# Kernel optimization log

Measured on AMD Instinct MI355X. Metric: run time of the kernel, lower is better.

## Reference

```python
import jax, jax.numpy as jnp
import numpy as np

B, N, E, D, M, T, P, HS, HN, C, NH = 64, 1024, 512, 1024, 16, 12, 2048, 2048, 64, 4, 8
EPS = 1e-8


def _ln(x, g, b):
    m = x.mean(-1, keepdims=True)
    v = ((x - m) ** 2).mean(-1, keepdims=True)
    return (x - m) / jnp.sqrt(v + 1e-5) * g + b


def _glu(x):
    a, b = jnp.split(x, 2, axis=-1)
    return a * jax.nn.sigmoid(b)


def setup_inputs() -> dict:
    key = jax.random.key(0)
    ks = jax.random.split(key, 24)
    s = 0.02
    rn = lambda k, sh: jax.random.normal(k, sh, jnp.float32) * s
    inp = {
        'kv_tokens': jax.random.normal(ks[0], (B, N, E), jnp.float32),
        'raw_r_act': jnp.full((P,), -10.0, jnp.float32),  # no_decay_init
        'raw_r_out': jnp.full((P,), -10.0, jnp.float32),
        'q_w': rn(ks[1], (E, P)), 'q_b': jnp.zeros((E,), jnp.float32),
        'in_proj_w': rn(ks[2], (3 * E, E)), 'in_proj_b': jnp.zeros((3 * E,), jnp.float32),
        'out_proj_w': rn(ks[3], (E, E)), 'out_proj_b': jnp.zeros((E,), jnp.float32),
        'z_ln_g': jnp.ones((D,), jnp.float32), 'z_ln_b': jnp.zeros((D,), jnp.float32),
        'o_ln_g': jnp.ones((E,), jnp.float32), 'o_ln_b': jnp.zeros((E,), jnp.float32),
        'gate_w': rn(ks[4], (D, D + E)), 'gate_b': jnp.zeros((D,), jnp.float32),
        'cand_w': rn(ks[5], (D, D + E)), 'cand_b': jnp.zeros((D,), jnp.float32),
        'syn1_w': rn(ks[6], (HS, D + E)), 'syn1_b': jnp.zeros((HS,), jnp.float32),
        'syn2_w': rn(ks[7], (D, HS)), 'syn2_b': jnp.zeros((D,), jnp.float32),
        'nlm1_w': rn(ks[8], (D, M, 2 * HN)), 'nlm1_b': jnp.zeros((D, 2 * HN), jnp.float32),
        'nlm2_w': rn(ks[9], (D, HN, 2)), 'nlm2_b': jnp.zeros((D, 2), jnp.float32),
        'head_w': rn(ks[10], (C, P)), 'head_b': jnp.zeros((C,), jnp.float32),
        'act_left': jax.random.randint(ks[11], (P,), 0, D),
        'act_right': jax.random.randint(ks[12], (P,), 0, D),
        'out_left': jax.random.randint(ks[13], (P,), 0, D),
        'out_right': jax.random.randint(ks[14], (P,), 0, D),
    }
    return inp


def reference(kv_tokens, raw_r_act, raw_r_out, q_w, q_b, in_proj_w, in_proj_b,
              out_proj_w, out_proj_b, z_ln_g, z_ln_b, o_ln_g, o_ln_b,
              gate_w, gate_b, cand_w, cand_b, syn1_w, syn1_b, syn2_w, syn2_b,
              nlm1_w, nlm1_b, nlm2_w, nlm2_b, head_w, head_b,
              act_left, act_right, out_left, out_right):
    dh = E // NH
    scale = 1.0 / np.sqrt(dh).astype(np.float32)
    Wq, Wk, Wv = jnp.split(in_proj_w, 3, axis=0)
    bq, bk, bv = jnp.split(in_proj_b, 3, axis=0)
    # K/V are tick-invariant: project once.
    k = (kv_tokens @ Wk.T + bk).reshape(B, N, NH, dh).transpose(0, 2, 1, 3)  # [B,H,N,dh]
    v = (kv_tokens @ Wv.T + bv).reshape(B, N, NH, dh).transpose(0, 2, 1, 3)
    decay_a = jnp.exp(-jax.nn.softplus(raw_r_act))[None, :]
    decay_o = jnp.exp(-jax.nn.softplus(raw_r_out))[None, :]

    z0 = jnp.zeros((B, D), kv_tokens.dtype)
    A0 = jnp.zeros((B, D, M), kv_tokens.dtype)
    # init_state with z0 == 0 -> alpha 0, beta 1, synch 0
    a_a0 = z0[:, act_left] * z0[:, act_right]
    b_a0 = jnp.ones_like(a_a0)
    s_a0 = a_a0 / jnp.sqrt(b_a0 + EPS)
    a_o0 = z0[:, out_left] * z0[:, out_right]
    b_o0 = jnp.ones_like(a_o0)

    def tick(carry, _):
        z, A, a_a, b_a, s_a, a_o, b_o = carry
        # attention query from action sync
        q = s_a @ q_w.T + q_b                                  # [B,E]
        qh = (q @ Wq.T + bq).reshape(B, NH, 1, dh)
        scores = jnp.einsum('bhqd,bhnd->bhqn', qh, k) * scale  # [B,H,1,N]
        attn = jax.nn.softmax(scores, axis=-1)
        o = jnp.einsum('bhqn,bhnd->bhqd', attn, v).reshape(B, E)
        o = o @ out_proj_w.T + out_proj_b
        o = _ln(o, o_ln_g, o_ln_b)                             # LN on o
        zn = _ln(z, z_ln_g, z_ln_b)                            # LN on z
        # gated fusion
        u = jnp.concatenate([zn, o], axis=-1)
        g = jax.nn.sigmoid(u @ gate_w.T + gate_b)
        h = jnp.tanh(u @ cand_w.T + cand_b)
        z_bar = (1.0 - g) * zn + g * h
        fused = jnp.concatenate([z_bar, o], axis=-1)           # [B,D+E]
        # synapse MLP -> pre-activation
        pre = jax.nn.gelu(fused @ syn1_w.T + syn1_b, approximate=False) @ syn2_w.T + syn2_b
        A = jnp.concatenate([A[:, :, 1:], pre[:, :, None]], axis=-1)  # shift history
        # deep NLM (per-neuron SuperLinear + GLU, twice)
        h1 = _glu(jnp.einsum('bdm,dmh->bdh', A, nlm1_w) + nlm1_b)
        z = _glu(jnp.einsum('bdh,dho->bdo', h1, nlm2_w) + nlm2_b)[..., 0]
        # decayed pair synchronisation updates
        a_a = decay_a * a_a + z[:, act_left] * z[:, act_right]
        b_a = decay_a * b_a + 1.0
        s_a = a_a / jnp.sqrt(b_a + EPS)
        a_o = decay_o * a_o + z[:, out_left] * z[:, out_right]
        b_o = decay_o * b_o + 1.0
        s_o = a_o / jnp.sqrt(b_o + EPS)
        logits = s_o @ head_w.T + head_b                       # [B,C]
        return (z, A, a_a, b_a, s_a, a_o, b_o), (logits, z)

    carry0 = (z0, A0, a_a0, b_a0, s_a0, a_o0, b_o0)
    _, (logits_t, z_t) = jax.lax.scan(tick, carry0, None, length=T)
    logits_ticks = jnp.transpose(logits_t, (1, 2, 0))          # [B,C,T]
    p = jnp.clip(jax.nn.softmax(logits_ticks, axis=1), 1e-8, None)
    ent = -(p * jnp.log(p)).sum(axis=1)
    certainty = 1.0 - ent / np.float32(np.log(C))              # [B,T]
    z_ticks = jnp.transpose(z_t, (1, 0, 2))                    # [B,T,D]
    return logits_ticks, certainty, z_ticks
```

## Files before the change

### kernel.cpp

```cpp
#include <hip/hip_runtime.h>
#include <hip/hip_bf16.h>

#define B_ 64
#define N_ 1024
#define E_ 512
#define D_ 1024
#define M_ 16
#define T_ 12
#define P_ 2048
#define HS_ 2048
#define HN_ 64
#define C_ 4
#define NH_ 8
#define DH_ 64

typedef __attribute__((ext_vector_type(8))) short bf16x8;
typedef __attribute__((ext_vector_type(4))) float f32x4;

__device__ __forceinline__ float bf2f(unsigned int u) {
    union { unsigned int i; float f; } c; c.i = (u & 0xffffu) << 16; return c.f;
}
__device__ __forceinline__ unsigned short f2bf(float f) {
    union { float f; unsigned int i; } c; c.f = f;
    unsigned int x = c.i;
    unsigned int r = x + 0x7fffu + ((x >> 16) & 1u);
    return (unsigned short)(r >> 16);
}

__global__ void init_kernel(unsigned short* s_a_bf, float* a_a, float* a_o, float* z) {
    int i = blockIdx.x * 256 + threadIdx.x;
    if (i < B_ * P_) { a_a[i] = 0.f; a_o[i] = 0.f; s_a_bf[i] = 0; }
    if (i < B_ * D_) z[i] = 0.f;
}

__global__ __launch_bounds__(256) void decay_prep_kernel(const float* __restrict__ raw_a,
                                                         const float* __restrict__ raw_o,
                                                         float* __restrict__ da, float* __restrict__ dz,
                                                         float* __restrict__ invsa, float* __restrict__ invso) {
    int p = blockIdx.x * 256 + threadIdx.x;
    if (p < P_) {
        float a = 1.f / (1.f + expf(raw_a[p]));
        float o = 1.f / (1.f + expf(raw_o[p]));
        da[p] = a; dz[p] = o;
        float ba = 1.f, bo = 1.f;
        for (int t = 0; t < T_; t++) {
            ba = a * ba + 1.f;
            bo = o * bo + 1.f;
            invsa[t * P_ + p] = 1.0f / sqrtf(ba + 1e-8f);
            invso[t * P_ + p] = 1.0f / sqrtf(bo + 1e-8f);
        }
    }
}

__global__ __launch_bounds__(256) void cvt_bf16_kernel(const float* __restrict__ in,
                                                       unsigned short* __restrict__ out, int n4) {
    int i = blockIdx.x * 256 + threadIdx.x;
    if (i < n4) {
        float4 v = ((const float4*)in)[i];
        ushort4 o;
        o.x = f2bf(v.x); o.y = f2bf(v.y); o.z = f2bf(v.z); o.w = f2bf(v.w);
        ((ushort4*)out)[i] = o;
    }
}

__global__ __launch_bounds__(256) void cvt_all_kernel(
    const float* s0, unsigned short* d0, int n0,
    const float* s1, unsigned short* d1, int n1,
    const float* s2, unsigned short* d2, int n2,
    const float* s3, unsigned short* d3, int n3,
    const float* s4, unsigned short* d4, int n4,
    const float* s5, unsigned short* d5, int n5) {
    int total = n0 + n1 + n2 + n3 + n4 + n5;
    for (int i = blockIdx.x * 256 + threadIdx.x; i < total; i += gridDim.x * 256) {
        const float* s; unsigned short* d; int j = i;
        if (j < n0) { s = s0; d = d0; }
        else { j -= n0;
        if (j < n1) { s = s1; d = d1; }
        else { j -= n1;
        if (j < n2) { s = s2; d = d2; }
        else { j -= n2;
        if (j < n3) { s = s3; d = d3; }
        else { j -= n3;
        if (j < n4) { s = s4; d = d4; }
        else { j -= n4; s = s5; d = d5; } } } } }
        float4 v = ((const float4*)s)[j];
        ushort4 o;
        o.x = f2bf(v.x); o.y = f2bf(v.y); o.z = f2bf(v.z); o.w = f2bf(v.w);
        ((ushort4*)d)[j] = o;
    }
}

__global__ __launch_bounds__(256) void cvt_ilv_kernel(const float* __restrict__ g,
                                                      const float* __restrict__ c,
                                                      unsigned short* __restrict__ out) {
    int r = blockIdx.x;
    const float* src = (r & 1) ? (c + (size_t)(r >> 1) * 1536) : (g + (size_t)(r >> 1) * 1536);
    for (int k = threadIdx.x * 4; k < 1536; k += 1024) {
        float4 v = *(const float4*)(src + k);
        ushort4 o;
        o.x = f2bf(v.x); o.y = f2bf(v.y); o.z = f2bf(v.z); o.w = f2bf(v.w);
        *(ushort4*)(out + (size_t)r * 1536 + k) = o;
    }
}

__global__ __launch_bounds__(256) void transpose_cvt_kernel(const float* __restrict__ in,
                                                            unsigned short* __restrict__ out,
                                                            int R, int Ccols) {
    __shared__ float tb[32][33];
    int c0 = blockIdx.x * 32, r0 = blockIdx.y * 32;
    int tx = threadIdx.x & 31, ty = threadIdx.x >> 5;
#pragma unroll
    for (int i = 0; i < 32; i += 8) tb[ty + i][tx] = in[(size_t)(r0 + ty + i) * Ccols + c0 + tx];
    __syncthreads();
#pragma unroll
    for (int i = 0; i < 32; i += 8) out[(size_t)(c0 + ty + i) * R + r0 + tx] = f2bf(tb[tx][ty + i]);
}

__global__ __launch_bounds__(256) void bcomb_kernel(const float* __restrict__ in_proj_w,
                                                    const float* __restrict__ in_proj_b,
                                                    const float* __restrict__ q_b,
                                                    float* __restrict__ bc) {
    int e = blockIdx.x * 256 + threadIdx.x;
    if (e < E_) {
        const float* wr = in_proj_w + (size_t)e * E_;
        float s = in_proj_b[e];
        for (int k = 0; k < E_; k += 4) {
            float4 w4 = *(const float4*)(wr + k);
            float4 q4 = *(const float4*)(q_b + k);
            s += w4.x * q4.x + w4.y * q4.y + w4.z * q4.z + w4.w * q4.w;
        }
        bc[e] = s;
    }
}

__global__ __launch_bounds__(256) void br_kernel(const float* __restrict__ in_proj_w,
                                                 const float* __restrict__ bc,
                                                 float* __restrict__ br) {
    int g = blockIdx.x * 256 + threadIdx.x;
    int h = g >> 9, j = g & 511;
    const float* Wk = in_proj_w + (size_t)E_ * E_;
    float s = 0.f;
    for (int e = 0; e < 64; e++) {
        s += Wk[(size_t)(h * 64 + e) * E_ + j] * bc[h * 64 + e];
    }
    br[g] = s;
}

template <bool HAS_BIAS>
__global__ __launch_bounds__(256) void gemm_bt_kernel(const unsigned short* __restrict__ A,
                                                      const unsigned short* __restrict__ Bt,
                                                      const float* __restrict__ bias,
                                                      unsigned short* __restrict__ C,
                                                      int M, int N, int K) {
    __shared__ __align__(16) unsigned short ldsA[2][4096];
    __shared__ __align__(16) unsigned short ldsB[2][4096];
    int id = blockIdx.y * gridDim.x + blockIdx.x;
    int nwg = gridDim.x * gridDim.y;
    int swz = (id & 7) * (nwg >> 3) + (id >> 3);
    int bx = swz % gridDim.x, by = swz / gridDim.x;
    int m0 = by * 128;
    int n0 = bx * 128;
    int tid = threadIdx.x;
    int wv = tid >> 6, l = tid & 63;
    int wr = wv >> 1, wc = wv & 1;
    int lr = l & 15, lg = l >> 4;
    f32x4 acc[4][4] = {};

    auto stage = [&](int buf, int kt) {
        int k0 = kt * 32;
#pragma unroll
        for (int i = 0; i < 2; i++) {
            int tsk = tid + 256 * i;
            int r = tsk >> 2, g = tsk & 3;
            int gs = (g ^ (r & 3)) * 8;
            __builtin_amdgcn_global_load_lds(
                (const __attribute__((address_space(1))) void*)(A + (size_t)(m0 + r) * K + k0 + gs),
                (__attribute__((address_space(3))) void*)&ldsA[buf][tsk * 8], 16, 0, 0);
        }
#pragma unroll
        for (int i = 0; i < 2; i++) {
            int tsk = tid + 256 * i;
            int r = tsk >> 2, g = tsk & 3;
            int gs = (g ^ (r & 3)) * 8;
            __builtin_amdgcn_global_load_lds(
                (const __attribute__((address_space(1))) void*)(Bt + (size_t)(n0 + r) * K + k0 + gs),
                (__attribute__((address_space(3))) void*)&ldsB[buf][tsk * 8], 16, 0, 0);
        }
    };

    int nt = K >> 5;
    stage(0, 0);
    for (int t = 0; t < nt; t++) {
        int cur = t & 1;
        if (t + 1 < nt) {
            stage(cur ^ 1, t + 1);
            asm volatile("s_waitcnt vmcnt(4)" ::: "memory");
        } else {
            asm volatile("s_waitcnt vmcnt(0)" ::: "memory");
        }
        __builtin_amdgcn_s_barrier();
        bf16x8 af[4], bfr[4];
#pragma unroll
        for (int mi = 0; mi < 4; mi++) {
            int r = wr * 64 + mi * 16 + lr;
            af[mi] = *(const bf16x8*)&ldsA[cur][r * 32 + ((lg ^ (r & 3)) << 3)];
        }
#pragma unroll
        for (int ni = 0; ni < 4; ni++) {
            int c = wc * 64 + ni * 16 + lr;
            bfr[ni] = *(const bf16x8*)&ldsB[cur][c * 32 + ((lg ^ (c & 3)) << 3)];
        }
#pragma unroll
        for (int mi = 0; mi < 4; mi++)
#pragma unroll
            for (int ni = 0; ni < 4; ni++)
                acc[mi][ni] = __builtin_amdgcn_mfma_f32_16x16x32_bf16(af[mi], bfr[ni], acc[mi][ni], 0, 0, 0);
        __builtin_amdgcn_s_barrier();
    }
#pragma unroll
    for (int ni = 0; ni < 4; ni++) {
        int col = n0 + wc * 64 + ni * 16 + lr;
        float bv = HAS_BIAS ? bias[col] : 0.0f;
#pragma unroll
        for (int mi = 0; mi < 4; mi++) {
            int row = m0 + wr * 64 + mi * 16 + lg * 4;
#pragma unroll
            for (int r = 0; r < 4; r++) {
                C[(size_t)(row + r) * N + col] = f2bf(acc[mi][ni][r] + bv);
            }
        }
    }
}

__global__ __launch_bounds__(256) void gemm_hb_kernel(const unsigned short* __restrict__ A0, int lda, size_t sAz,
                                                      const unsigned short* __restrict__ B0, int ldb, size_t sBz,
                                                      unsigned short* __restrict__ C0, int ldc, size_t sCz,
                                                      int K) {
    __shared__ __align__(16) unsigned short ldsA[2][4096];
    __shared__ __align__(16) unsigned short ldsB[2][4096];
    const unsigned short* A = A0 + blockIdx.z * sAz;
    const unsigned short* Bt = B0 + blockIdx.z * sBz;
    unsigned short* C = C0 + blockIdx.z * sCz;
    int m0 = blockIdx.y * 128, n0 = blockIdx.x * 128;
    int tid = threadIdx.x;
    int wv = tid >> 6, l = tid & 63;
    int wr = wv >> 1, wc = wv & 1;
    int lr = l & 15, lg = l >> 4;
    f32x4 acc[4][4] = {};

    auto stage = [&](int buf, int kt) {
        int k0 = kt * 32;
#pragma unroll
        for (int i = 0; i < 2; i++) {
            int tsk = tid + 256 * i;
            int r = tsk >> 2, g = tsk & 3;
            int gs = (g ^ (r & 3)) * 8;
            __builtin_amdgcn_global_load_lds(
                (const __attribute__((address_space(1))) void*)(A + (size_t)(m0 + r) * lda + k0 + gs),
                (__attribute__((address_space(3))) void*)&ldsA[buf][tsk * 8], 16, 0, 0);
        }
#pragma unroll
        for (int i = 0; i < 2; i++) {
            int tsk = tid + 256 * i;
            int r = tsk >> 2, g = tsk & 3;
            int gs = (g ^ (r & 3)) * 8;
            __builtin_amdgcn_global_load_lds(
                (const __attribute__((address_space(1))) void*)(Bt + (size_t)(n0 + r) * ldb + k0 + gs),
                (__attribute__((address_space(3))) void*)&ldsB[buf][tsk * 8], 16, 0, 0);
        }
    };

    int nt = K >> 5;
    stage(0, 0);
    for (int t = 0; t < nt; t++) {
        int cur = t & 1;
        if (t + 1 < nt) {
            stage(cur ^ 1, t + 1);
            asm volatile("s_waitcnt vmcnt(4)" ::: "memory");
        } else {
            asm volatile("s_waitcnt vmcnt(0)" ::: "memory");
        }
        __builtin_amdgcn_s_barrier();
        bf16x8 af[4], bfr[4];
#pragma unroll
        for (int mi = 0; mi < 4; mi++) {
            int r = wr * 64 + mi * 16 + lr;
            af[mi] = *(const bf16x8*)&ldsA[cur][r * 32 + ((lg ^ (r & 3)) << 3)];
        }
#pragma unroll
        for (int ni = 0; ni < 4; ni++) {
            int c = wc * 64 + ni * 16 + lr;
            bfr[ni] = *(const bf16x8*)&ldsB[cur][c * 32 + ((lg ^ (c & 3)) << 3)];
        }
#pragma unroll
        for (int mi = 0; mi < 4; mi++)
#pragma unroll
            for (int ni = 0; ni < 4; ni++)
                acc[mi][ni] = __builtin_amdgcn_mfma_f32_16x16x32_bf16(af[mi], bfr[ni], acc[mi][ni], 0, 0, 0);
        __builtin_amdgcn_s_barrier();
    }
#pragma unroll
    for (int ni = 0; ni < 4; ni++) {
        int col = n0 + wc * 64 + ni * 16 + lr;
#pragma unroll
        for (int mi = 0; mi < 4; mi++) {
            int row = m0 + wr * 64 + mi * 16 + lg * 4;
#pragma unroll
            for (int r = 0; r < 4; r++) {
                C[(size_t)(row + r) * ldc + col] = f2bf(acc[mi][ni][r]);
            }
        }
    }
}

template <int EPI>
__global__ __launch_bounds__(256) void gemmNK_kernel(const unsigned short* __restrict__ A,
                                                     const unsigned short* __restrict__ W,
                                                     const float* __restrict__ bias0,
                                                     const float* __restrict__ bias1,
                                                     const float* __restrict__ zn32,
                                                     void* __restrict__ outp,
                                                     int N, int K) {
    __shared__ __align__(16) unsigned short ldsA[4][2][2048];
    __shared__ __align__(16) unsigned short ldsB[4][2][512];
    int n0 = blockIdx.x * 16;
    int tid = threadIdx.x;
    int w = tid >> 6, l = tid & 63;
    int Kw = K >> 2;
    int kb = w * Kw;
    int lr = l & 15, lg = l >> 4;
    int ar = l >> 2, ag = l & 3;
    f32x4 acc[4] = {};

    auto stage = [&](int buf, int kt) {
        int k0 = kb + (kt << 5);
#pragma unroll
        for (int i = 0; i < 4; i++) {
            int row = i * 16 + ar;
            int gs = (ag ^ (row & 3)) << 3;
            __builtin_amdgcn_global_load_lds(
                (const __attribute__((address_space(1))) void*)(A + (size_t)row * K + k0 + gs),
                (__attribute__((address_space(3))) void*)&ldsA[w][buf][i * 512 + l * 8], 16, 0, 0);
        }
        {
            int col = ar;
            int gs = (ag ^ (col & 3)) << 3;
            __builtin_amdgcn_global_load_lds(
                (const __attribute__((address_space(1))) void*)(W + (size_t)(n0 + col) * K + k0 + gs),
                (__attribute__((address_space(3))) void*)&ldsB[w][buf][l * 8], 16, 0, 0);
        }
    };

    int nt = Kw >> 5;
    stage(0, 0);
    for (int t = 0; t < nt; t++) {
        int cur = t & 1;
        if (t + 1 < nt) {
            stage(cur ^ 1, t + 1);
            asm volatile("s_waitcnt vmcnt(5)" ::: "memory");
        } else {
            asm volatile("s_waitcnt vmcnt(0)" ::: "memory");
        }
        bf16x8 bf = *(const bf16x8*)&ldsB[w][cur][lr * 32 + ((lg ^ (lr & 3)) << 3)];
#pragma unroll
        for (int mi = 0; mi < 4; mi++) {
            int rr = mi * 16 + lr;
            bf16x8 af = *(const bf16x8*)&ldsA[w][cur][rr * 32 + ((lg ^ (rr & 3)) << 3)];
            acc[mi] = __builtin_amdgcn_mfma_f32_16x16x32_bf16(af, bf, acc[mi], 0, 0, 0);
        }
    }
    __syncthreads();
    float* red = (float*)&ldsA[0][0][0];
#pragma unroll
    for (int mi = 0; mi < 4; mi++) {
        int row = mi * 16 + lg * 4;
#pragma unroll
        for (int q = 0; q < 4; q++) red[w * 1024 + (row + q) * 16 + lr] = acc[mi][q];
    }
    __syncthreads();
    int b = tid >> 2, c4 = (tid & 3) << 2;
    f32x4 s = *(f32x4*)&red[b * 16 + c4];
#pragma unroll
    for (int ww = 1; ww < 4; ww++) {
        f32x4 v = *(f32x4*)&red[ww * 1024 + b * 16 + c4];
        s[0] += v[0]; s[1] += v[1]; s[2] += v[2]; s[3] += v[3];
    }
    int col = n0 + c4;
    if (EPI == 0) {
        unsigned short* out = (unsigned short*)outp;
        ushort4 o;
        o.x = f2bf(0.125f * (s[0] + bias0[col + 0]));
        o.y = f2bf(0.125f * (s[1] + bias0[col + 1]));
        o.z = f2bf(0.125f * (s[2] + bias0[col + 2]));
        o.w = f2bf(0.125f * (s[3] + bias0[col + 3]));
        *(ushort4*)(out + (size_t)b * N + col) = o;
    } else if (EPI == 1) {
        float* out = (float*)outp;
        *(f32x4*)(out + (size_t)b * N + col) = s;
    } else if (EPI == 2) {
        unsigned short* out = (unsigned short*)outp;
        int j0 = col >> 1;
#pragma unroll
        for (int pp = 0; pp < 2; pp++) {
            int j = j0 + pp;
            float g = 1.0f / (1.0f + expf(-(s[pp * 2] + bias0[j])));
            float h = tanhf(s[pp * 2 + 1] + bias1[j]);
            float zb = (1.0f - g) * zn32[(size_t)b * D_ + j] + g * h;
            out[(size_t)b * 1536 + j] = f2bf(zb);
        }
    } else if (EPI == 3) {
        unsigned short* out = (unsigned short*)outp;
        ushort4 o;
#pragma unroll
        for (int j = 0; j < 4; j++) {
            float pre = s[j] + bias0[col + j];
            float val = 0.5f * pre * (1.0f + erff(pre * 0.70710678118654752f));
            ((unsigned short*)&o)[j] = f2bf(val);
        }
        *(ushort4*)(out + (size_t)b * N + col) = o;
    } else {
        float* out = (float*)outp;
#pragma unroll
        for (int j = 0; j < 4; j++) {
            out[(size_t)(col + j) * 64 + b] = s[j] + bias0[col + j];
        }
    }
}

__global__ __launch_bounds__(256) void scoreX_kernel(const unsigned short* __restrict__ X,
                                                     const unsigned short* __restrict__ r_bf,
                                                     float* __restrict__ S) {
    int b = blockIdx.y;
    int n0 = blockIdx.x * 128;
    int tid = threadIdx.x;
    int wv = tid >> 6, l = tid & 63;
    int lr = l & 15, lg = l >> 4;
    const unsigned short* Xb = X + ((size_t)b * 1024 + n0) * 512;
    const unsigned short* rb = r_bf + (size_t)b * 4096 + (size_t)(lr & 7) * 512 + lg * 8;
    f32x4 acc[2] = {};
#pragma unroll
    for (int kt = 0; kt < 16; kt++) {
        int k0 = kt * 32;
        bf16x8 bfrag = *(const bf16x8*)(rb + k0);
#pragma unroll
        for (int mi = 0; mi < 2; mi++) {
            int row = (wv * 2 + mi) * 16 + lr;
            bf16x8 afrag = *(const bf16x8*)(Xb + (size_t)row * 512 + k0 + lg * 8);
            acc[mi] = __builtin_amdgcn_mfma_f32_16x16x32_bf16(afrag, bfrag, acc[mi], 0, 0, 0);
        }
    }
    if (lr < 8) {
#pragma unroll
        for (int mi = 0; mi < 2; mi++) {
            int rowbase = (wv * 2 + mi) * 16 + lg * 4;
#pragma unroll
            for (int q = 0; q < 4; q++) {
                S[((size_t)b * 8 + lr) * 1024 + n0 + rowbase + q] = acc[mi][q];
            }
        }
    }
}

__global__ __launch_bounds__(256) void attnV_kernel(const float* __restrict__ S,
                                                    const unsigned short* __restrict__ vbuf,
                                                    unsigned short* __restrict__ o_bf) {
    int bh = blockIdx.x;
    int b = bh >> 3, h = bh & 7;
    __shared__ float sc[N_];
    __shared__ float red[8];
    __shared__ float opart[4][DH_];
    int tid = threadIdx.x;
    int w = tid >> 6, lane = tid & 63;
    const float* Ss = S + ((size_t)b * 8 + h) * 1024;
    float myv[4];
#pragma unroll
    for (int i = 0; i < 4; i++) myv[i] = Ss[tid + i * 256];
    float m = fmaxf(fmaxf(myv[0], myv[1]), fmaxf(myv[2], myv[3]));
#pragma unroll
    for (int off = 32; off >= 1; off >>= 1) m = fmaxf(m, __shfl_xor(m, off, 64));
    if (lane == 0) red[w] = m;
    __syncthreads();
    m = fmaxf(fmaxf(red[0], red[1]), fmaxf(red[2], red[3]));
    float s = 0.f;
#pragma unroll
    for (int i = 0; i < 4; i++) {
        float e = expf(myv[i] - m);
        sc[tid + i * 256] = e;
        s += e;
    }
#pragma unroll
    for (int off = 32; off >= 1; off >>= 1) s += __shfl_xor(s, off, 64);
    if (lane == 0) red[4 + w] = s;
    __syncthreads();
    float inv = 1.0f / (red[4] + red[5] + red[6] + red[7]);
    const unsigned short* vb = vbuf + (size_t)b * 1024 * 512 + h * DH_;
    int ng = lane >> 4, d4 = (lane & 15) << 2;
    float a0 = 0.f, a1 = 0.f, a2 = 0.f, a3 = 0.f;
    int n0 = w * 256;
    for (int i = 0; i < 64; i++) {
        int n = n0 + i * 4 + ng;
        uint2 pv = *(const uint2*)(vb + (size_t)n * 512 + d4);
        float sv = sc[n];
        a0 += sv * bf2f(pv.x);
        a1 += sv * bf2f(pv.x >> 16);
        a2 += sv * bf2f(pv.y);
        a3 += sv * bf2f(pv.y >> 16);
    }
    a0 += __shfl_xor(a0, 16, 64); a0 += __shfl_xor(a0, 32, 64);
    a1 += __shfl_xor(a1, 16, 64); a1 += __shfl_xor(a1, 32, 64);
    a2 += __shfl_xor(a2, 16, 64); a2 += __shfl_xor(a2, 32, 64);
    a3 += __shfl_xor(a3, 16, 64); a3 += __shfl_xor(a3, 32, 64);
    if (lane < 16) {
        opart[w][d4 + 0] = a0;
        opart[w][d4 + 1] = a1;
        opart[w][d4 + 2] = a2;
        opart[w][d4 + 3] = a3;
    }
    __syncthreads();
    if (tid < DH_) {
        float r = (opart[0][tid] + opart[1][tid] + opart[2][tid] + opart[3][tid]) * inv;
        o_bf[(size_t)b * E_ + h * DH_ + tid] = f2bf(r);
    }
}

__global__ __launch_bounds__(256) void reduce_oln_kernel(const float* __restrict__ opre,
                                                         const float* __restrict__ bout,
                                                         const float* __restrict__ og,
                                                         const float* __restrict__ obv,
                                                         const float* __restrict__ z,
                                                         const float* __restrict__ zg,
                                                         const float* __restrict__ zbv,
                                                         unsigned short* __restrict__ u_bf,
                                                         unsigned short* __restrict__ fused_bf,
                                                         float* __restrict__ zn32) {
    int b = blockIdx.x, tid = threadIdx.x;
    __shared__ float red[16];
    float v[2];
#pragma unroll
    for (int i = 0; i < 2; i++) {
        int e = tid + i * 256;
        v[i] = opre[(size_t)b * E_ + e] + bout[e];
    }
    int w = tid >> 6, lane = tid & 63;
    float s1 = v[0] + v[1];
    float s2 = v[0] * v[0] + v[1] * v[1];
#pragma unroll
    for (int off = 32; off >= 1; off >>= 1) { s1 += __shfl_xor(s1, off, 64); s2 += __shfl_xor(s2, off, 64); }
    if (lane == 0) { red[w] = s1; red[4 + w] = s2; }
    __syncthreads();
    s1 = red[0] + red[1] + red[2] + red[3];
    s2 = red[4] + red[5] + red[6] + red[7];
    float mean = s1 * (1.0f / 512.0f);
    float var = s2 * (1.0f / 512.0f) - mean * mean;
    float rstd = 1.0f / sqrtf(var + 1e-5f);
#pragma unroll
    for (int i = 0; i < 2; i++) {
        int e = tid + i * 256;
        unsigned short val = f2bf((v[i] - mean) * rstd * og[e] + obv[e]);
        u_bf[(size_t)b * 1536 + D_ + e] = val;
        fused_bf[(size_t)b * 1536 + D_ + e] = val;
    }
    float zl[4];
    float t1 = 0.f, t2 = 0.f;
#pragma unroll
    for (int i = 0; i < 4; i++) {
        int d = tid + i * 256;
        zl[i] = z[(size_t)b * D_ + d];
        t1 += zl[i]; t2 += zl[i] * zl[i];
    }
#pragma unroll
    for (int off = 32; off >= 1; off >>= 1) { t1 += __shfl_xor(t1, off, 64); t2 += __shfl_xor(t2, off, 64); }
    __syncthreads();
    if (lane == 0) { red[8 + w] = t1; red[12 + w] = t2; }
    __syncthreads();
    t1 = red[8] + red[9] + red[10] + red[11];
    t2 = red[12] + red[13] + red[14] + red[15];
    float zmean = t1 * (1.0f / 1024.0f);
    float zvar = t2 * (1.0f / 1024.0f) - zmean * zmean;
    float zr = 1.0f / sqrtf(zvar + 1e-5f);
#pragma unroll
    for (int i = 0; i < 4; i++) {
        int d = tid + i * 256;
        float zn = (zl[i] - zmean) * zr * zg[d] + zbv[d];
        u_bf[(size_t)b * 1536 + d] = f2bf(zn);
        zn32[(size_t)b * D_ + d] = zn;
    }
}

template <int NT>
__global__ __launch_bounds__(256) void nlm_kernel(const float* __restrict__ AbufT,
                                                  const unsigned short* __restrict__ w1g_bf,
                                                  const float* __restrict__ b1g,
                                                  const float* __restrict__ w2g,
                                                  const float* __restrict__ b2g,
                                                  float* __restrict__ z,
                                                  float* __restrict__ zt) {
    __shared__ float w1s[4][2048];
    __shared__ float b1s[4][128];
    __shared__ float w2s[4][128];
    __shared__ float b2s[4][2];
    int tid = threadIdx.x;
    int w = tid >> 6, lane = tid & 63;
    int d = blockIdx.x * 4 + w;
    for (int i = lane * 2; i < 2048; i += 128) {
        unsigned int pk = *(const unsigned int*)(w1g_bf + (size_t)d * 2048 + i);
        w1s[w][i] = bf2f(pk);
        w1s[w][i + 1] = bf2f(pk >> 16);
    }
    for (int i = lane; i < 128; i += 64) {
        b1s[w][i] = b1g[(size_t)d * 128 + i];
        w2s[w][i] = w2g[(size_t)d * 128 + i];
    }
    if (lane < 2) b2s[w][lane] = b2g[d * 2 + lane];
    __syncthreads();
    const int b = lane;
    float av[NT];
#pragma unroll
    for (int s = 0; s < NT; s++) av[s] = AbufT[((size_t)s * D_ + d) * 64 + b];
    constexpr int moff = M_ - NT;
    float o0 = b2s[w][0], o1 = b2s[w][1];
    for (int hh = 0; hh < 64; hh++) {
        float a = b1s[w][hh], bb = b1s[w][hh + 64];
#pragma unroll
        for (int s = 0; s < NT; s++) {
            float x = av[s];
            a += x * w1s[w][(s + moff) * 128 + hh];
            bb += x * w1s[w][(s + moff) * 128 + hh + 64];
        }
        float z1 = a / (1.0f + expf(-bb));
        o0 += z1 * w2s[w][hh * 2];
        o1 += z1 * w2s[w][hh * 2 + 1];
    }
    float zv = o0 / (1.0f + expf(-o1));
    z[(size_t)b * D_ + d] = zv;
    zt[((size_t)b * T_ + (NT - 1)) * D_ + d] = zv;
}

__global__ __launch_bounds__(256) void synchead_kernel(const float* __restrict__ z,
                                                       const int* __restrict__ act_l, const int* __restrict__ act_r,
                                                       const int* __restrict__ out_l, const int* __restrict__ out_r,
                                                       const float* __restrict__ da, const float* __restrict__ dz,
                                                       const float* __restrict__ invsa_t, const float* __restrict__ invso_t,
                                                       const float* __restrict__ head_w, const float* __restrict__ head_b,
                                                       float* __restrict__ a_a,
                                                       unsigned short* __restrict__ s_a_bf,
                                                       float* __restrict__ a_o,
                                                       float* __restrict__ out_logits, float* __restrict__ out_cert, int t) {
    int b = blockIdx.x, tid = threadIdx.x;
    __shared__ float zv[D_];
    __shared__ float red[4][4];
    for (int i = tid; i < D_; i += 256) zv[i] = z[(size_t)b * D_ + i];
    __syncthreads();
    float l0 = 0.f, l1 = 0.f, l2 = 0.f, l3 = 0.f;
    for (int p = tid; p < P_; p += 256) {
        size_t ip = (size_t)b * P_ + p;
        float aa = da[p] * a_a[ip] + zv[act_l[p]] * zv[act_r[p]];
        a_a[ip] = aa;
        s_a_bf[(size_t)b * P_ + p] = f2bf(aa * invsa_t[p]);
        float ao = dz[p] * a_o[ip] + zv[out_l[p]] * zv[out_r[p]];
        a_o[ip] = ao;
        float so = ao * invso_t[p];
        l0 += so * head_w[p];
        l1 += so * head_w[P_ + p];
        l2 += so * head_w[2 * P_ + p];
        l3 += so * head_w[3 * P_ + p];
    }
    int w = tid >> 6, lane = tid & 63;
#pragma unroll
    for (int off = 32; off >= 1; off >>= 1) {
        l0 += __shfl_xor(l0, off, 64);
        l1 += __shfl_xor(l1, off, 64);
        l2 += __shfl_xor(l2, off, 64);
        l3 += __shfl_xor(l3, off, 64);
    }
    if (lane == 0) { red[w][0] = l0; red[w][1] = l1; red[w][2] = l2; red[w][3] = l3; }
    __syncthreads();
    if (tid == 0) {
        float lg[4];
#pragma unroll
        for (int c = 0; c < 4; c++) {
            lg[c] = red[0][c] + red[1][c] + red[2][c] + red[3][c] + head_b[c];
            out_logits[((size_t)b * C_ + c) * T_ + t] = lg[c];
        }
        float m = fmaxf(fmaxf(lg[0], lg[1]), fmaxf(lg[2], lg[3]));
        float e0 = expf(lg[0] - m), e1 = expf(lg[1] - m), e2 = expf(lg[2] - m), e3 = expf(lg[3] - m);
        float inv = 1.0f / (e0 + e1 + e2 + e3);
        float ent = 0.f, pp;
        pp = fmaxf(e0 * inv, 1e-8f); ent -= pp * logf(pp);
        pp = fmaxf(e1 * inv, 1e-8f); ent -= pp * logf(pp);
        pp = fmaxf(e2 * inv, 1e-8f); ent -= pp * logf(pp);
        pp = fmaxf(e3 * inv, 1e-8f); ent -= pp * logf(pp);
        out_cert[(size_t)b * T_ + t] = 1.0f - ent * (1.0f / 1.3862943611198906f);
    }
}

extern "C" void kernel_launch(void* const* d_in, const int* in_sizes, int n_in,
                              void* d_out, int out_size, void* d_ws, size_t ws_size,
                              hipStream_t stream) {
    const float* kv_tokens  = (const float*)d_in[0];
    const float* raw_r_act  = (const float*)d_in[1];
    const float* raw_r_out  = (const float*)d_in[2];
    const float* q_w        = (const float*)d_in[3];
    const float* q_b        = (const float*)d_in[4];
    const float* in_proj_w  = (const float*)d_in[5];
    const float* in_proj_b  = (const float*)d_in[6];
    const float* out_proj_w = (const float*)d_in[7];
    const float* out_proj_b = (const float*)d_in[8];
    const float* z_ln_g     = (const float*)d_in[9];
    const float* z_ln_b     = (const float*)d_in[10];
    const float* o_ln_g     = (const float*)d_in[11];
    const float* o_ln_b     = (const float*)d_in[12];
    const float* gate_w     = (const float*)d_in[13];
    const float* gate_b     = (const float*)d_in[14];
    const float* cand_w     = (const float*)d_in[15];
    const float* cand_b     = (const float*)d_in[16];
    const float* syn1_w     = (const float*)d_in[17];
    const float* syn1_b     = (const float*)d_in[18];
    const float* syn2_w     = (const float*)d_in[19];
    const float* syn2_b     = (const float*)d_in[20];
    const float* nlm1_w     = (const float*)d_in[21];
    const float* nlm1_b     = (const float*)d_in[22];
    const float* nlm2_w     = (const float*)d_in[23];
    const float* nlm2_b     = (const float*)d_in[24];
    const float* head_w     = (const float*)d_in[25];
    const float* head_b     = (const float*)d_in[26];
    const int* act_l        = (const int*)d_in[27];
    const int* act_r        = (const int*)d_in[28];
    const int* out_l        = (const int*)d_in[29];
    const int* out_r        = (const int*)d_in[30];

    float* out = (float*)d_out;
    float* out_logits = out;
    float* out_cert = out + B_ * C_ * T_;
    float* out_zt = out_cert + B_ * T_;

    char* ws = (char*)d_ws;
    size_t off = 0;
    auto alloc = [&](size_t bytes) { void* p = ws + off; off += (bytes + 255) & ~(size_t)255; return p; };
    unsigned short* kv_bf   = (unsigned short*)alloc((size_t)B_ * N_ * E_ * 2);
    unsigned short* vbuf    = (unsigned short*)alloc((size_t)B_ * N_ * E_ * 2);
    unsigned short* Wv_bf   = (unsigned short*)alloc((size_t)E_ * E_ * 2);
    unsigned short* Wq_bf   = (unsigned short*)alloc((size_t)E_ * E_ * 2);
    unsigned short* WkT_bf  = (unsigned short*)alloc((size_t)E_ * E_ * 2);
    unsigned short* qwT_bf  = (unsigned short*)alloc((size_t)P_ * E_ * 2);
    unsigned short* WcT_bf  = (unsigned short*)alloc((size_t)P_ * E_ * 2);
    unsigned short* Gmat    = (unsigned short*)alloc((size_t)4096 * P_ * 2);
    unsigned short* Wgc_bf  = (unsigned short*)alloc((size_t)2048 * 1536 * 2);
    unsigned short* Ws1_bf  = (unsigned short*)alloc((size_t)2048 * 1536 * 2);
    unsigned short* Ws2_bf  = (unsigned short*)alloc((size_t)1024 * 2048 * 2);
    unsigned short* Wout_bf = (unsigned short*)alloc((size_t)E_ * E_ * 2);
    unsigned short* nlm1w_bf= (unsigned short*)alloc((size_t)1024 * 2048 * 2);
    float* bc   = (float*)alloc(E_ * 4);
    float* brv  = (float*)alloc(4096 * 4);
    float* da   = (float*)alloc(P_ * 4);
    float* dzv  = (float*)alloc(P_ * 4);
    float* invsa = (float*)alloc((size_t)T_ * P_ * 4);
    float* invso = (float*)alloc((size_t)T_ * P_ * 4);
    unsigned short* s_a_bf  = (unsigned short*)alloc((size_t)B_ * P_ * 2);
    unsigned short* r_bf    = (unsigned short*)alloc((size_t)B_ * 4096 * 2);
    float* Sbuf = (float*)alloc((size_t)B_ * 8 * N_ * 4);
    unsigned short* o_bf    = (unsigned short*)alloc((size_t)B_ * E_ * 2);
    unsigned short* u_bf    = (unsigned short*)alloc((size_t)B_ * 1536 * 2);
    unsigned short* fused_bf= (unsigned short*)alloc((size_t)B_ * 1536 * 2);
    unsigned short* tbuf_bf = (unsigned short*)alloc((size_t)B_ * HS_ * 2);
    float* opre = (float*)alloc((size_t)B_ * E_ * 4);
    float* zn32 = (float*)alloc((size_t)B_ * D_ * 4);
    float* a_a  = (float*)alloc((size_t)B_ * P_ * 4);
    float* a_o  = (float*)alloc((size_t)B_ * P_ * 4);
    float* zbuf = (float*)alloc((size_t)B_ * D_ * 4);
    float* AbufT = (float*)alloc((size_t)T_ * D_ * B_ * 4);

    init_kernel<<<512, 256, 0, stream>>>(s_a_bf, a_a, a_o, zbuf);
    decay_prep_kernel<<<8, 256, 0, stream>>>(raw_r_act, raw_r_out, da, dzv, invsa, invso);

    cvt_bf16_kernel<<<(B_ * N_ * E_ / 4) / 256, 256, 0, stream>>>(kv_tokens, kv_bf, B_ * N_ * E_ / 4);
    cvt_all_kernel<<<2048, 256, 0, stream>>>(
        in_proj_w + (size_t)2 * E_ * E_, Wv_bf, E_ * E_ / 4,
        in_proj_w, Wq_bf, E_ * E_ / 4,
        out_proj_w, Wout_bf, E_ * E_ / 4,
        syn1_w, Ws1_bf, 2048 * 1536 / 4,
        syn2_w, Ws2_bf, 1024 * 2048 / 4,
        nlm1_w, nlm1w_bf, 1024 * 2048 / 4);
    cvt_ilv_kernel<<<2048, 256, 0, stream>>>(gate_w, cand_w, Wgc_bf);
    transpose_cvt_kernel<<<dim3(16, 16), 256, 0, stream>>>(in_proj_w + (size_t)E_ * E_, WkT_bf, E_, E_);
    transpose_cvt_kernel<<<dim3(P_ / 32, E_ / 32), 256, 0, stream>>>(q_w, qwT_bf, E_, P_);
    bcomb_kernel<<<2, 256, 0, stream>>>(in_proj_w, in_proj_b, q_b, bc);
    br_kernel<<<16, 256, 0, stream>>>(in_proj_w, bc, brv);
    gemm_bt_kernel<false><<<dim3(E_ / 128, P_ / 128), 256, 0, stream>>>(qwT_bf, Wq_bf, nullptr, WcT_bf, P_, E_, E_);
    gemm_hb_kernel<<<dim3(P_ / 128, E_ / 128, NH_), 256, 0, stream>>>(WkT_bf, E_, 64,
                                                                      WcT_bf, E_, 64,
                                                                      Gmat, P_, (size_t)512 * P_, 64);
    gemm_bt_kernel<true><<<dim3(E_ / 128, B_ * N_ / 128), 256, 0, stream>>>(kv_bf, Wv_bf, in_proj_b + 2 * E_,
                                                                            vbuf, B_ * N_, E_, E_);

    for (int t = 0; t < T_; t++) {
        gemmNK_kernel<0><<<256, 256, 0, stream>>>(s_a_bf, Gmat, brv, nullptr, nullptr, r_bf, 4096, P_);
        scoreX_kernel<<<dim3(8, 64), 256, 0, stream>>>(kv_bf, r_bf, Sbuf);
        attnV_kernel<<<B_ * NH_, 256, 0, stream>>>(Sbuf, vbuf, o_bf);
        gemmNK_kernel<1><<<32, 256, 0, stream>>>(o_bf, Wout_bf, nullptr, nullptr, nullptr, opre, E_, E_);
        reduce_oln_kernel<<<64, 256, 0, stream>>>(opre, out_proj_b, o_ln_g, o_ln_b,
                                                  zbuf, z_ln_g, z_ln_b, u_bf, fused_bf, zn32);
        gemmNK_kernel<2><<<128, 256, 0, stream>>>(u_bf, Wgc_bf, gate_b, cand_b, zn32, fused_bf, 2048, 1536);
        gemmNK_kernel<3><<<128, 256, 0, stream>>>(fused_bf, Ws1_bf, syn1_b, nullptr, nullptr, tbuf_bf, 2048, 1536);
        gemmNK_kernel<4><<<64, 256, 0, stream>>>(tbuf_bf, Ws2_bf, syn2_b, nullptr, nullptr,
                                                 AbufT + (size_t)t * D_ * 64, 1024, 2048);
        switch (t) {
            case 0:  nlm_kernel<1><<<256, 256, 0, stream>>>(AbufT, nlm1w_bf, nlm1_b, nlm2_w, nlm2_b, zbuf, out_zt); break;
            case 1:  nlm_kernel<2><<<256, 256, 0, stream>>>(AbufT, nlm1w_bf, nlm1_b, nlm2_w, nlm2_b, zbuf, out_zt); break;
            case 2:  nlm_kernel<3><<<256, 256, 0, stream>>>(AbufT, nlm1w_bf, nlm1_b, nlm2_w, nlm2_b, zbuf, out_zt); break;
            case 3:  nlm_kernel<4><<<256, 256, 0, stream>>>(AbufT, nlm1w_bf, nlm1_b, nlm2_w, nlm2_b, zbuf, out_zt); break;
            case 4:  nlm_kernel<5><<<256, 256, 0, stream>>>(AbufT, nlm1w_bf, nlm1_b, nlm2_w, nlm2_b, zbuf, out_zt); break;
            case 5:  nlm_kernel<6><<<256, 256, 0, stream>>>(AbufT, nlm1w_bf, nlm1_b, nlm2_w, nlm2_b, zbuf, out_zt); break;
            case 6:  nlm_kernel<7><<<256, 256, 0, stream>>>(AbufT, nlm1w_bf, nlm1_b, nlm2_w, nlm2_b, zbuf, out_zt); break;
            case 7:  nlm_kernel<8><<<256, 256, 0, stream>>>(AbufT, nlm1w_bf, nlm1_b, nlm2_w, nlm2_b, zbuf, out_zt); break;
            case 8:  nlm_kernel<9><<<256, 256, 0, stream>>>(AbufT, nlm1w_bf, nlm1_b, nlm2_w, nlm2_b, zbuf, out_zt); break;
            case 9:  nlm_kernel<10><<<256, 256, 0, stream>>>(AbufT, nlm1w_bf, nlm1_b, nlm2_w, nlm2_b, zbuf, out_zt); break;
            case 10: nlm_kernel<11><<<256, 256, 0, stream>>>(AbufT, nlm1w_bf, nlm1_b, nlm2_w, nlm2_b, zbuf, out_zt); break;
            default: nlm_kernel<12><<<256, 256, 0, stream>>>(AbufT, nlm1w_bf, nlm1_b, nlm2_w, nlm2_b, zbuf, out_zt); break;
        }
        synchead_kernel<<<64, 256, 0, stream>>>(zbuf, act_l, act_r, out_l, out_r, da, dzv,
                                                invsa + t * P_, invso + t * P_,
                                                head_w, head_b, a_a, s_a_bf, a_o,
                                                out_logits, out_cert, t);
    }
}
```

Baseline: 1.292 ms.

## Widen V-projection GEMM tile, vectorize attnV loads, skip first-tick r GEMM

```diff
diff --git a/kernel.cpp b/kernel.cpp
--- a/kernel.cpp
+++ b/kernel.cpp
@@ -27,27 +27,23 @@
     return (unsigned short)(r >> 16);
 }
 
-__global__ void init_kernel(unsigned short* s_a_bf, float* a_a, float* a_o, float* z) {
+__global__ void init_kernel(unsigned short* s_a_bf, float* a_a, float* a_o, float* z,
+                            const float* __restrict__ raw_a, const float* __restrict__ raw_o,
+                            float* __restrict__ da, float* __restrict__ dz,
+                            float* __restrict__ invsa, float* __restrict__ invso) {
     int i = blockIdx.x * 256 + threadIdx.x;
     if (i < B_ * P_) { a_a[i] = 0.f; a_o[i] = 0.f; s_a_bf[i] = 0; }
     if (i < B_ * D_) z[i] = 0.f;
-}
-
-__global__ __launch_bounds__(256) void decay_prep_kernel(const float* __restrict__ raw_a,
-                                                         const float* __restrict__ raw_o,
-                                                         float* __restrict__ da, float* __restrict__ dz,
-                                                         float* __restrict__ invsa, float* __restrict__ invso) {
-    int p = blockIdx.x * 256 + threadIdx.x;
-    if (p < P_) {
-        float a = 1.f / (1.f + expf(raw_a[p]));
-        float o = 1.f / (1.f + expf(raw_o[p]));
-        da[p] = a; dz[p] = o;
+    if (i < P_) {
+        float a = 1.f / (1.f + expf(raw_a[i]));
+        float o = 1.f / (1.f + expf(raw_o[i]));
+        da[i] = a; dz[i] = o;
         float ba = 1.f, bo = 1.f;
         for (int t = 0; t < T_; t++) {
             ba = a * ba + 1.f;
             bo = o * bo + 1.f;
-            invsa[t * P_ + p] = 1.0f / sqrtf(ba + 1e-8f);
-            invso[t * P_ + p] = 1.0f / sqrtf(bo + 1e-8f);
+            invsa[t * P_ + i] = 1.0f / sqrtf(ba + 1e-8f);
+            invso[t * P_ + i] = 1.0f / sqrtf(bo + 1e-8f);
         }
     }
 }
@@ -146,6 +142,14 @@
     br[g] = s;
 }
 
+__global__ __launch_bounds__(256) void r0_kernel(const float* __restrict__ brv,
+                                                 unsigned short* __restrict__ r_bf) {
+    int i = blockIdx.x * 256 + threadIdx.x;
+    if (i < B_ * 4096) {
+        r_bf[i] = f2bf(0.125f * brv[i & 4095]);
+    }
+}
+
 template <bool HAS_BIAS>
 __global__ __launch_bounds__(256) void gemm_bt_kernel(const unsigned short* __restrict__ A,
                                                       const unsigned short* __restrict__ Bt,
@@ -232,6 +236,91 @@
     }
 }
 
+__global__ __launch_bounds__(256) void gemm_bt_wide_kernel(const unsigned short* __restrict__ A,
+                                                           const unsigned short* __restrict__ Bt,
+                                                           const float* __restrict__ bias,
+                                                           unsigned short* __restrict__ C,
+                                                           int M, int N, int K) {
+    __shared__ __align__(16) unsigned short ldsA[2][4096];
+    __shared__ __align__(16) unsigned short ldsB[2][8192];
+    int id = blockIdx.y * gridDim.x + blockIdx.x;
+    int nwg = gridDim.x * gridDim.y;
+    int swz = (id & 7) * (nwg >> 3) + (id >> 3);
+    int bx = swz % gridDim.x, by = swz / gridDim.x;
+    int m0 = by * 128;
+    int n0 = bx * 256;
+    int tid = threadIdx.x;
+    int wv = tid >> 6, l = tid & 63;
+    int wr = wv >> 1, wc = wv & 1;
+    int lr = l & 15, lg = l >> 4;
+    f32x4 acc[4][8] = {};
+
+    auto stage = [&](int buf, int kt) {
+        int k0 = kt * 32;
+#pragma unroll
+        for (int i = 0; i < 2; i++) {
+            int tsk = tid + 256 * i;
+            int r = tsk >> 2, g = tsk & 3;
+            int gs = (g ^ (r & 3)) * 8;
+            __builtin_amdgcn_global_load_lds(
+                (const __attribute__((address_space(1))) void*)(A + (size_t)(m0 + r) * K + k0 + gs),
+                (__attribute__((address_space(3))) void*)&ldsA[buf][tsk * 8], 16, 0, 0);
+        }
+#pragma unroll
+        for (int i = 0; i < 4; i++) {
+            int tsk = tid + 256 * i;
+            int r = tsk >> 2, g = tsk & 3;
+            int gs = (g ^ (r & 3)) * 8;
+            __builtin_amdgcn_global_load_lds(
+                (const __attribute__((address_space(1))) void*)(Bt + (size_t)(n0 + r) * K + k0 + gs),
+                (__attribute__((address_space(3))) void*)&ldsB[buf][tsk * 8], 16, 0, 0);
+        }
+    };
+
+    int nt = K >> 5;
+    stage(0, 0);
+    for (int t = 0; t < nt; t++) {
+        int cur = t & 1;
+        if (t + 1 < nt) {
+            stage(cur ^ 1, t + 1);
+            asm volatile("s_waitcnt vmcnt(6)" ::: "memory");
+        } else {
+            asm volatile("s_waitcnt vmcnt(0)" ::: "memory");
+        }
+        __builtin_amdgcn_s_barrier();
+        bf16x8 af[4], bfr[8];
+#pragma unroll
+        for (int mi = 0; mi < 4; mi++) {
+            int r = wr * 64 + mi * 16 + lr;
+            af[mi] = *(const bf16x8*)&ldsA[cur][r * 32 + ((lg ^ (r & 3)) << 3)];
+        }
+#pragma unroll
+        for (int ni = 0; ni < 8; ni++) {
+            int c = wc * 128 + ni * 16 + lr;
+            bfr[ni] = *(const bf16x8*)&ldsB[cur][c * 32 + ((lg ^ (c & 3)) << 3)];
+        }
+#pragma unroll
+        for (int mi = 0; mi < 4; mi++)
+#pragma unroll
+            for (int ni = 0; ni < 8; ni++)
+                acc[mi][ni] = __builtin_amdgcn_mfma_f32_16x16x32_bf16(af[mi], bfr[ni], acc[mi][ni], 0, 0, 0);
+        __builtin_amdgcn_s_barrier();
+    }
+#pragma unroll
+    for (int ni = 0; ni < 8; ni++) {
+        int col = n0 + wc * 128 + ni * 16 + lr;
+        float bv = bias[col];
+#pragma unroll
+        for (int mi = 0; mi < 4; mi++) {
+            int row = m0 + wr * 64 + mi * 16 + lg * 4;
+#pragma unroll
+            for (int r = 0; r < 4; r++) {
+                C[(size_t)(row + r) * N + col] = f2bf(acc[mi][ni][r] + bv);
+            }
+        }
+    }
+}
+
 __global__ __launch_bounds__(256) void gemm_hb_kernel(const unsigned short* __restrict__ A0, int lda, size_t sAz,
                                                       const unsigned short* __restrict__ B0, int ldb, size_t sBz,
                                                       unsigned short* __restrict__ C0, int ldc, size_t sCz,
@@ -494,27 +583,31 @@
     __syncthreads();
     float inv = 1.0f / (red[4] + red[5] + red[6] + red[7]);
     const unsigned short* vb = vbuf + (size_t)b * 1024 * 512 + h * DH_;
-    int ng = lane >> 4, d4 = (lane & 15) << 2;
-    float a0 = 0.f, a1 = 0.f, a2 = 0.f, a3 = 0.f;
+    int ng = lane >> 3, d8 = (lane & 7) << 3;
+    float a[8] = {};
     int n0 = w * 256;
-    for (int i = 0; i < 64; i++) {
-        int n = n0 + i * 4 + ng;
-        uint2 pv = *(const uint2*)(vb + (size_t)n * 512 + d4);
+    for (int i = 0; i < 32; i++) {
+        int n = n0 + i * 8 + ng;
+        uint4 pv = *(const uint4*)(vb + (size_t)n * 512 + d8);
         float sv = sc[n];
-        a0 += sv * bf2f(pv.x);
-        a1 += sv * bf2f(pv.x >> 16);
-        a2 += sv * bf2f(pv.y);
-        a3 += sv * bf2f(pv.y >> 16);
-    }
-    a0 += __shfl_xor(a0, 16, 64); a0 += __shfl_xor(a0, 32, 64);
-    a1 += __shfl_xor(a1, 16, 64); a1 += __shfl_xor(a1, 32, 64);
-    a2 += __shfl_xor(a2, 16, 64); a2 += __shfl_xor(a2, 32, 64);
-    a3 += __shfl_xor(a3, 16, 64); a3 += __shfl_xor(a3, 32, 64);
-    if (lane < 16) {
-        opart[w][d4 + 0] = a0;
-        opart[w][d4 + 1] = a1;
-        opart[w][d4 + 2] = a2;
-        opart[w][d4 + 3] = a3;
+        a[0] += sv * bf2f(pv.x);
+        a[1] += sv * bf2f(pv.x >> 16);
+        a[2] += sv * bf2f(pv.y);
+        a[3] += sv * bf2f(pv.y >> 16);
+        a[4] += sv * bf2f(pv.z);
+        a[5] += sv * bf2f(pv.z >> 16);
+        a[6] += sv * bf2f(pv.w);
+        a[7] += sv * bf2f(pv.w >> 16);
+    }
+#pragma unroll
+    for (int j = 0; j < 8; j++) {
+        a[j] += __shfl_xor(a[j], 8, 64);
+        a[j] += __shfl_xor(a[j], 16, 64);
+        a[j] += __shfl_xor(a[j], 32, 64);
+    }
+    if (lane < 8) {
+#pragma unroll
+        for (int j = 0; j < 8; j++) opart[w][d8 + j] = a[j];
     }
     __syncthreads();
     if (tid < DH_) {
@@ -770,8 +863,8 @@
     float* zbuf = (float*)alloc((size_t)B_ * D_ * 4);
     float* AbufT = (float*)alloc((size_t)T_ * D_ * B_ * 4);
 
-    init_kernel<<<512, 256, 0, stream>>>(s_a_bf, a_a, a_o, zbuf);
-    decay_prep_kernel<<<8, 256, 0, stream>>>(raw_r_act, raw_r_out, da, dzv, invsa, invso);
+    init_kernel<<<512, 256, 0, stream>>>(s_a_bf, a_a, a_o, zbuf,
+                                         raw_r_act, raw_r_out, da, dzv, invsa, invso);
 
     cvt_bf16_kernel<<<(B_ * N_ * E_ / 4) / 256, 256, 0, stream>>>(kv_tokens, kv_bf, B_ * N_ * E_ / 4);
     cvt_all_kernel<<<2048, 256, 0, stream>>>(
@@ -786,15 +879,18 @@
     transpose_cvt_kernel<<<dim3(P_ / 32, E_ / 32), 256, 0, stream>>>(q_w, qwT_bf, E_, P_);
     bcomb_kernel<<<2, 256, 0, stream>>>(in_proj_w, in_proj_b, q_b, bc);
     br_kernel<<<16, 256, 0, stream>>>(in_proj_w, bc, brv);
+    r0_kernel<<<(B_ * 4096) / 256, 256, 0, stream>>>(brv, r_bf);
     gemm_bt_kernel<false><<<dim3(E_ / 128, P_ / 128), 256, 0, stream>>>(qwT_bf, Wq_bf, nullptr, WcT_bf, P_, E_, E_);
     gemm_hb_kernel<<<dim3(P_ / 128, E_ / 128, NH_), 256, 0, stream>>>(WkT_bf, E_, 64,
                                                                       WcT_bf, E_, 64,
                                                                       Gmat, P_, (size_t)512 * P_, 64);
-    gemm_bt_kernel<true><<<dim3(E_ / 128, B_ * N_ / 128), 256, 0, stream>>>(kv_bf, Wv_bf, in_proj_b + 2 * E_,
-                                                                            vbuf, B_ * N_, E_, E_);
+    gemm_bt_wide_kernel<<<dim3(E_ / 256, B_ * N_ / 128), 256, 0, stream>>>(kv_bf, Wv_bf, in_proj_b + 2 * E_,
+                                                                           vbuf, B_ * N_, E_, E_);
 
     for (int t = 0; t < T_; t++) {
-        gemmNK_kernel<0><<<256, 256, 0, stream>>>(s_a_bf, Gmat, brv, nullptr, nullptr, r_bf, 4096, P_);
+        if (t > 0) {
+            gemmNK_kernel<0><<<256, 256, 0, stream>>>(s_a_bf, Gmat, brv, nullptr, nullptr, r_bf, 4096, P_);
+        }
         scoreX_kernel<<<dim3(8, 64), 256, 0, stream>>>(kv_bf, r_bf, Sbuf);
         attnV_kernel<<<B_ * NH_, 256, 0, stream>>>(Sbuf, vbuf, o_bf);
         gemmNK_kernel<1><<<32, 256, 0, stream>>>(o_bf, Wout_bf, nullptr, nullptr, nullptr, opre, E_, E_);
```

Result: slower. 1.330 ms (+3.0%).
